# Kernel optimization log

Hardware: AMD Instinct MI355X
Metric: run time of the kernel (lower is better)

## Reference

```python
import jax, jax.numpy as jnp
import numpy as np
from jax import lax

P = 8  # patch size
DN = ('NCHW', 'OIHW', 'NCHW')

def setup_inputs() -> dict:
    key = jax.random.key(0)
    ks = jax.random.split(key, 8)
    B, D, H, W = 8, 64, 256, 256
    C = 4 * D
    return {
        'x': jax.random.normal(ks[0], (B, D, H, W), jnp.float32),
        'w_in': jax.random.normal(ks[1], (C, D, 1, 1), jnp.float32) * 0.05,
        'b_in': jax.random.normal(ks[2], (C,), jnp.float32) * 0.05,
        'fft_filter': jnp.ones((C, 1, 1, P, P // 2 + 1), jnp.float32),
        'w_dw': jax.random.normal(ks[3], (C, 1, 7, 7), jnp.float32) * 0.05,
        'b_dw': jax.random.normal(ks[4], (C,), jnp.float32) * 0.05,
        'w_out': jax.random.normal(ks[5], (D, C, 1, 1), jnp.float32) * 0.05,
        'b_out': jax.random.normal(ks[6], (D,), jnp.float32) * 0.05,
    }

def reference(x, w_in, b_in, fft_filter, w_dw, b_dw, w_out, b_out):
    B, D, H, W = x.shape
    C = w_in.shape[0]
    # conv_in: 1x1
    x = lax.conv_general_dilated(x, w_in, (1, 1), 'SAME', dimension_numbers=DN)
    x = x + b_in[None, :, None, None]
    # patchify: b c (h p1) (w p2) -> b c h w p1 p2
    xp = x.reshape(B, C, H // P, P, W // P, P).transpose(0, 1, 2, 4, 3, 5)
    # rfft2 over 8x8 patches (norm='backward' is default)
    xf = jnp.fft.rfft2(xp)
    # learned frequency filter (real), broadcasts over batch and patch grid
    xf = xf * fft_filter
    xp = jnp.fft.irfft2(xf, s=(P, P))
    # unpatchify
    x = xp.transpose(0, 1, 2, 4, 3, 5).reshape(B, C, H, W)
    # depthwise 7x7 conv
    x = lax.conv_general_dilated(x, w_dw, (1, 1), 'SAME',
                                 dimension_numbers=DN, feature_group_count=C)
    x = x + b_dw[None, :, None, None]
    x = jax.nn.gelu(x, approximate=False)
    # conv3: 1x1 back to dim
    x = lax.conv_general_dilated(x, w_out, (1, 1), 'SAME', dimension_numbers=DN)
    return x + b_out[None, :, None, None]
```

## Files before the change

kernel.cpp:

```cpp
#include <hip/hip_runtime.h>
#include <cstdint>
#include <cstddef>

#define HWSZ 65536

__device__ __forceinline__ uint32_t f2bfu(float f) {
  union { float f; uint32_t u; } v; v.f = f;
  return (v.u + 0x7FFFu + ((v.u >> 16) & 1u)) >> 16;
}
__device__ __forceinline__ float bfhi(uint32_t u) {
  union { uint32_t u; float f; } v; v.u = u & 0xffff0000u;
  return v.f;
}
__device__ __forceinline__ float bflo(uint32_t u) {
  union { uint32_t u; float f; } v; v.u = u << 16;
  return v.f;
}

__global__ void k_prep(const float* __restrict__ F, float* __restrict__ Ks) {
  __shared__ float ct[8];
  int t = threadIdx.x;
  int c = blockIdx.x;
  if (t == 0) {
    const float r2 = 0.70710678118654752f;
    ct[0] = 1.f; ct[1] = r2; ct[2] = 0.f; ct[3] = -r2;
    ct[4] = -1.f; ct[5] = -r2; ct[6] = 0.f; ct[7] = r2;
  }
  __syncthreads();
  int p = t >> 3, q = t & 7;
  const float* Fc = F + c * 40;
  float s = 0.f;
#pragma unroll
  for (int u = 0; u < 8; ++u) {
#pragma unroll
    for (int v = 0; v < 8; ++v) {
      float g = (v <= 4) ? Fc[u * 5 + v] : Fc[((8 - u) & 7) * 5 + (8 - v)];
      s += g * ct[(u * p + v * q) & 7];
    }
  }
  Ks[c * 64 + t] = s * (1.f / 64.f);
}

__global__ void k_wt(const float* __restrict__ w_out, float* __restrict__ wT) {
  int c = blockIdx.x;
  int d = threadIdx.x;
  wT[c * 64 + d] = w_out[d * 256 + c];
}

__global__ void k_wdw(const float* __restrict__ w_dw,
                      const float* __restrict__ b_dw,
                      float* __restrict__ wdwp) {
  int c = blockIdx.x;
  int t = threadIdx.x;
  int u = t >> 3, k = t & 7;
  float v = 0.f;
  if (t == 55) v = b_dw[c];
  else if (t < 56 && k < 7) v = w_dw[c * 49 + u * 7 + k];
  wdwp[c * 64 + t] = v;
}

__device__ __forceinline__ void circ8(const uint32_t* __restrict__ prb,
                                      const float* __restrict__ kc, int h,
                                      uint32_t* __restrict__ ou) {
  float o[32];
#pragma unroll
  for (int t = 0; t < 32; ++t) o[t] = 0.f;
#pragma unroll 1
  for (int tph = 0; tph < 2; ++tph) {
    float kh[32];
#pragma unroll
    for (int q4 = 0; q4 < 8; ++q4) {
      float4 kv = *(const float4*)(kc + tph * 32 + q4 * 4);
      kh[q4 * 4 + 0] = kv.x; kh[q4 * 4 + 1] = kv.y;
      kh[q4 * 4 + 2] = kv.z; kh[q4 * 4 + 3] = kv.w;
    }
#pragma unroll
    for (int ii = 0; ii < 4; ++ii) {
      int i = h * 4 + ii;
#pragma unroll
      for (int t4 = 0; t4 < 4; ++t4) {
        int tp = tph * 4 + t4;
        int r = (i - tp) & 7;
        uint2 ua = *(const uint2*)(prb + r * 4);
        uint2 ub = *(const uint2*)(prb + r * 4 + 2);
        float pr[8] = {bflo(ua.x), bfhi(ua.x), bflo(ua.y), bfhi(ua.y),
                       bflo(ub.x), bfhi(ub.x), bflo(ub.y), bfhi(ub.y)};
#pragma unroll
        for (int tq = 0; tq < 8; ++tq) {
          float kv = kh[t4 * 8 + tq];
#pragma unroll
          for (int j = 0; j < 8; ++j)
            o[ii * 8 + j] += kv * pr[(j - tq) & 7];
        }
      }
    }
  }
#pragma unroll
  for (int ii = 0; ii < 4; ++ii) {
    ou[ii * 4 + 0] = f2bfu(o[ii * 8 + 0]) | (f2bfu(o[ii * 8 + 1]) << 16);
    ou[ii * 4 + 1] = f2bfu(o[ii * 8 + 2]) | (f2bfu(o[ii * 8 + 3]) << 16);
    ou[ii * 4 + 2] = f2bfu(o[ii * 8 + 4]) | (f2bfu(o[ii * 8 + 5]) << 16);
    ou[ii * 4 + 3] = f2bfu(o[ii * 8 + 6]) | (f2bfu(o[ii * 8 + 7]) << 16);
  }
}

__global__ __launch_bounds__(256, 2) void k_front(
    const float* __restrict__ x, const float* __restrict__ w_in,
    const float* __restrict__ b_in, const float* __restrict__ Ks,
    uint32_t* __restrict__ midu) {
  __shared__ __align__(16) uint32_t Au[128 * 34];
  __shared__ __align__(16) uint32_t Bu[128 * 34];
  float* xs = (float*)Au;
  int tid = threadIdx.x;
  int orig = blockIdx.x;
  int pid = (orig & 7) * 1024 + (orig >> 3);
  int b = pid >> 10;
  int pp = pid & 1023;
  int ph = pp >> 5, pw = pp & 31;

  {
    const float* xb = x + (size_t)b * 64 * HWSZ + (ph * 8) * 256 + pw * 8;
#pragma unroll
    for (int k = 0; k < 4; ++k) {
      int s = tid + k * 256;
      int d = s >> 4, i = (s >> 1) & 7, jh = s & 1;
      float4 v = *(const float4*)(xb + (size_t)d * HWSZ + i * 256 + jh * 4);
      *(float4*)(xs + d * 64 + i * 8 + jh * 4) = v;
    }
  }
  int h = tid & 1;
  int cp = tid >> 1;
  int c0 = cp, c1 = cp + 128;
  float p0[32], p1[32];
  {
    float bi0 = b_in[c0], bi1 = b_in[c1];
#pragma unroll
    for (int t = 0; t < 32; ++t) { p0[t] = bi0; p1[t] = bi1; }
  }
  __syncthreads();

  const float* w0 = w_in + c0 * 64;
  const float* w1 = w_in + c1 * 64;
#pragma unroll 1
  for (int d8 = 0; d8 < 8; ++d8) {
    float4 wa0 = *(const float4*)(w0 + d8 * 8);
    float4 wb0 = *(const float4*)(w0 + d8 * 8 + 4);
    float4 wa1 = *(const float4*)(w1 + d8 * 8);
    float4 wb1 = *(const float4*)(w1 + d8 * 8 + 4);
    float wv0[8] = {wa0.x, wa0.y, wa0.z, wa0.w, wb0.x, wb0.y, wb0.z, wb0.w};
    float wv1[8] = {wa1.x, wa1.y, wa1.z, wa1.w, wb1.x, wb1.y, wb1.z, wb1.w};
#pragma unroll
    for (int dd = 0; dd < 8; ++dd) {
      const float4* xr = (const float4*)(xs + (d8 * 8 + dd) * 64 + h * 32);
#pragma unroll
      for (int t4 = 0; t4 < 8; ++t4) {
        float4 xv = xr[t4];
        p0[t4 * 4 + 0] += wv0[dd] * xv.x; p1[t4 * 4 + 0] += wv1[dd] * xv.x;
        p0[t4 * 4 + 1] += wv0[dd] * xv.y; p1[t4 * 4 + 1] += wv1[dd] * xv.y;
        p0[t4 * 4 + 2] += wv0[dd] * xv.z; p1[t4 * 4 + 2] += wv1[dd] * xv.z;
        p0[t4 * 4 + 3] += wv0[dd] * xv.w; p1[t4 * 4 + 3] += wv1[dd] * xv.w;
      }
    }
  }
  __syncthreads();

  {
    uint32_t* r0 = Au + c0 * 34 + h * 16;
    uint32_t* r1 = Bu + cp * 34 + h * 16;
#pragma unroll
    for (int ii = 0; ii < 4; ++ii) {
      uint2 ua, ub;
      ua.x = f2bfu(p0[ii * 8 + 0]) | (f2bfu(p0[ii * 8 + 1]) << 16);
      ua.y = f2bfu(p0[ii * 8 + 2]) | (f2bfu(p0[ii * 8 + 3]) << 16);
      ub.x = f2bfu(p0[ii * 8 + 4]) | (f2bfu(p0[ii * 8 + 5]) << 16);
      ub.y = f2bfu(p0[ii * 8 + 6]) | (f2bfu(p0[ii * 8 + 7]) << 16);
      *(uint2*)(r0 + ii * 4) = ua;
      *(uint2*)(r0 + ii * 4 + 2) = ub;
      ua.x = f2bfu(p1[ii * 8 + 0]) | (f2bfu(p1[ii * 8 + 1]) << 16);
      ua.y = f2bfu(p1[ii * 8 + 2]) | (f2bfu(p1[ii * 8 + 3]) << 16);
      ub.x = f2bfu(p1[ii * 8 + 4]) | (f2bfu(p1[ii * 8 + 5]) << 16);
      ub.y = f2bfu(p1[ii * 8 + 6]) | (f2bfu(p1[ii * 8 + 7]) << 16);
      *(uint2*)(r1 + ii * 4) = ua;
      *(uint2*)(r1 + ii * 4 + 2) = ub;
    }
  }
  __syncthreads();

  uint32_t ou[16];
  circ8(Au + c0 * 34, Ks + c0 * 64, h, ou);
  __syncthreads();
  {
    uint32_t* r0 = Au + c0 * 34 + h * 16;
#pragma unroll
    for (int m = 0; m < 4; ++m) {
      uint2 ua; ua.x = ou[m * 4 + 0]; ua.y = ou[m * 4 + 1];
      uint2 ub; ub.x = ou[m * 4 + 2]; ub.y = ou[m * 4 + 3];
      *(uint2*)(r0 + m * 4) = ua;
      *(uint2*)(r0 + m * 4 + 2) = ub;
    }
  }
  circ8(Bu + cp * 34, Ks + c1 * 64, h, ou);
  __syncthreads();
  {
    uint32_t* r1 = Bu + cp * 34 + h * 16;
#pragma unroll
    for (int m = 0; m < 4; ++m) {
      uint2 ua; ua.x = ou[m * 4 + 0]; ua.y = ou[m * 4 + 1];
      uint2 ub; ub.x = ou[m * 4 + 2]; ub.y = ou[m * 4 + 3];
      *(uint2*)(r1 + m * 4) = ua;
      *(uint2*)(r1 + m * 4 + 2) = ub;
    }
  }
  __syncthreads();

  uint32_t* gbase = midu + (size_t)(b * 1024 + pp) * 8192;
#pragma unroll
  for (int k = 0; k < 8; ++k) {
    int g = tid * 4 + k * 1024;
    int w = g & 31;
    uint2 a, e;
    if (k < 4) {
      int cc = g >> 5;
      a = *(uint2*)(Au + cc * 34 + w);
      e = *(uint2*)(Au + cc * 34 + w + 2);
    } else {
      int cc = (g >> 5) - 128;
      a = *(uint2*)(Bu + cc * 34 + w);
      e = *(uint2*)(Bu + cc * 34 + w + 2);
    }
    uint4 q; q.x = a.x; q.y = a.y; q.z = e.x; q.w = e.y;
    *(uint4*)(gbase + g) = q;
  }
}

#define TUB 48
__global__ __launch_bounds__(256, 1) void k_back(
    const uint32_t* __restrict__ midu, const float* __restrict__ wdwp,
    const float* __restrict__ wT, const float* __restrict__ b_out,
    float* __restrict__ out) {
  __shared__ __align__(16) uint32_t tile[2][22 * TUB];
  __shared__ __align__(16) float wbuf[2][128];
  int t = threadIdx.x;
  int orig = blockIdx.x;
  int pid = (orig & 7) * 128 + (orig >> 3);
  int b = pid >> 7;
  int tb = pid & 127;
  int th = tb >> 3, tw = tb & 7;
  int R0 = th * 16, C0 = tw * 32;

  for (int z = t; z < 2 * 22 * TUB; z += 256) ((uint32_t*)tile)[z] = 0u;

  int lr = t >> 3, p = t & 7;
  int g = R0 - 3 + lr;
  int pc = 4 * tw - 1 + p;
  bool aw = (t < 176) && (p < 6) && ((unsigned)g < 256u);
  bool qv = aw && ((unsigned)pc < 32u);
  size_t src0 = 0;
  if (qv)
    src0 = ((size_t)(b * 1024 + (g >> 3) * 32 + pc) * 8192) +
           (size_t)((g & 7) * 4);

  int ty = t >> 4, tx = t & 15;
  int lane = t - 192;

  float2 acc[64];
#pragma unroll
  for (int d = 0; d < 64; ++d) { acc[d].x = 0.f; acc[d].y = 0.f; }

  __syncthreads();

  {
    uint4 q; q.x = 0u; q.y = 0u; q.z = 0u; q.w = 0u;
    if (qv) q = *(const uint4*)(midu + src0);
    uint32_t ex = (uint32_t)__shfl_down((int)q.x, 1);
    if (aw) {
      uint32_t* dr = &tile[0][0] + lr * TUB;
      uint32_t w0 = (q.x >> 16) | (q.y << 16);
      uint32_t w1 = (q.y >> 16) | (q.z << 16);
      uint32_t w2 = (q.z >> 16) | (q.w << 16);
      uint32_t w3 = (q.w >> 16) | (ex << 16);
      if (p == 0) {
        uint2 hb; hb.x = w2; hb.y = w3;
        *(uint2*)(dr + 0) = hb;
      } else if (p == 5) {
        dr[18] = w0;
      } else {
        uint2 ha; ha.x = w0; ha.y = w1;
        uint2 hb; hb.x = w2; hb.y = w3;
        *(uint2*)(dr + 4 * p - 2) = ha;
        *(uint2*)(dr + 4 * p) = hb;
      }
    }
    if (t >= 192) {
      __builtin_amdgcn_global_load_lds(
          (const __attribute__((address_space(1))) uint32_t*)(wdwp + lane),
          (__attribute__((address_space(3))) uint32_t*)&wbuf[0][0], 4, 0, 0);
      __builtin_amdgcn_global_load_lds(
          (const __attribute__((address_space(1))) uint32_t*)(wT + lane),
          (__attribute__((address_space(3))) uint32_t*)&wbuf[0][64], 4, 0, 0);
    }
  }
  __syncthreads();

  for (int c = 0; c < 256; ++c) {
    int cur = c & 1;
    bool pf = (c < 255);
    uint4 q; q.x = 0u; q.y = 0u; q.z = 0u; q.w = 0u;
    if (pf && qv) q = *(const uint4*)(midu + src0 + (size_t)(c + 1) * 32);
    if (pf && t >= 192) {
      const float* wds = wdwp + (size_t)(c + 1) * 64 + lane;
      const float* wts = wT + (size_t)(c + 1) * 64 + lane;
      __builtin_amdgcn_global_load_lds(
          (const __attribute__((address_space(1))) uint32_t*)wds,
          (__attribute__((address_space(3))) uint32_t*)&wbuf[cur ^ 1][0],
          4, 0, 0);
      __builtin_amdgcn_global_load_lds(
          (const __attribute__((address_space(1))) uint32_t*)wts,
          (__attribute__((address_space(3))) uint32_t*)&wbuf[cur ^ 1][64],
          4, 0, 0);
    }

    const uint32_t* tl = &tile[cur][0];
    const float* wl = wbuf[cur];
    float s0 = wl[55], s1 = s0;
#pragma unroll
    for (int u = 0; u < 7; ++u) {
      const uint32_t* row = tl + (ty + u) * TUB + tx;
      uint32_t k0 = row[0], k1 = row[1], k2 = row[2], k3 = row[3];
      float f0 = bflo(k0), f1 = bfhi(k0), f2 = bflo(k1), f3 = bfhi(k1);
      float f4 = bflo(k2), f5 = bfhi(k2), f6 = bflo(k3), f7 = bfhi(k3);
      float4 wA = *(const float4*)(wl + u * 8);
      float4 wB = *(const float4*)(wl + u * 8 + 4);
      s0 += wA.x * f0 + wA.y * f1 + wA.z * f2 + wA.w * f3 + wB.x * f4 +
            wB.y * f5 + wB.z * f6;
      s1 += wA.x * f1 + wA.y * f2 + wA.z * f3 + wA.w * f4 + wB.x * f5 +
            wB.y * f6 + wB.z * f7;
    }
    const float RS2 = 0.70710678118654752f;
    float g0 = 0.5f * s0 * (1.f + erff(s0 * RS2));
    float g1 = 0.5f * s1 * (1.f + erff(s1 * RS2));

    const float* wcl = wl + 64;
#pragma unroll
    for (int d4 = 0; d4 < 16; ++d4) {
      float4 wv = *(const float4*)(wcl + d4 * 4);
      acc[d4 * 4 + 0].x += g0 * wv.x; acc[d4 * 4 + 0].y += g1 * wv.x;
      acc[d4 * 4 + 1].x += g0 * wv.y; acc[d4 * 4 + 1].y += g1 * wv.y;
      acc[d4 * 4 + 2].x += g0 * wv.z; acc[d4 * 4 + 2].y += g1 * wv.z;
      acc[d4 * 4 + 3].x += g0 * wv.w; acc[d4 * 4 + 3].y += g1 * wv.w;
    }

    if (pf) {
      uint32_t ex = (uint32_t)__shfl_down((int)q.x, 1);
      if (aw) {
        uint32_t* dr = &tile[cur ^ 1][0] + lr * TUB;
        uint32_t w0 = (q.x >> 16) | (q.y << 16);
        uint32_t w1 = (q.y >> 16) | (q.z << 16);
        uint32_t w2 = (q.z >> 16) | (q.w << 16);
        uint32_t w3 = (q.w >> 16) | (ex << 16);
        if (p == 0) {
          uint2 hb; hb.x = w2; hb.y = w3;
          *(uint2*)(dr + 0) = hb;
        } else if (p == 5) {
          dr[18] = w0;
        } else {
          uint2 ha; ha.x = w0; ha.y = w1;
          uint2 hb; hb.x = w2; hb.y = w3;
          *(uint2*)(dr + 4 * p - 2) = ha;
          *(uint2*)(dr + 4 * p) = hb;
        }
      }
    }
    __syncthreads();
  }

  size_t obase = (size_t)b * 64 * HWSZ + (size_t)(R0 + ty) * 256 + C0 + 2 * tx;
#pragma unroll
  for (int d = 0; d < 64; ++d) {
    float bo = b_out[d];
    float2 v; v.x = acc[d].x + bo; v.y = acc[d].y + bo;
    *(float2*)(out + obase + (size_t)d * HWSZ) = v;
  }
}

extern "C" void kernel_launch(void* const* d_in, const int* in_sizes, int n_in,
                              void* d_out, int out_size, void* d_ws, size_t ws_size,
                              hipStream_t stream) {
  (void)in_sizes; (void)n_in; (void)out_size; (void)ws_size;
  const float* x     = (const float*)d_in[0];
  const float* w_in  = (const float*)d_in[1];
  const float* b_in  = (const float*)d_in[2];
  const float* fftf  = (const float*)d_in[3];
  const float* w_dw  = (const float*)d_in[4];
  const float* b_dw  = (const float*)d_in[5];
  const float* w_out = (const float*)d_in[6];
  const float* b_out = (const float*)d_in[7];
  float* out = (float*)d_out;

  float* Ks = (float*)d_ws;
  float* wT = (float*)((char*)d_ws + 65536);
  float* wdwp = (float*)((char*)d_ws + 131072);
  uint32_t* midu = (uint32_t*)((char*)d_ws + 196608);

  k_prep<<<256, 64, 0, stream>>>(fftf, Ks);
  k_wt<<<256, 64, 0, stream>>>(w_out, wT);
  k_wdw<<<256, 64, 0, stream>>>(w_dw, b_dw, wdwp);
  k_front<<<8192, 256, 0, stream>>>(x, w_in, b_in, Ks, midu);
  k_back<<<1024, 256, 0, stream>>>(midu, wdwp, wT, b_out, out);
}
```

Baseline: 1.381 ms.

## Stream back-kernel tiles via async global-to-LDS loads with 8-deep channel ring

Replaces the register-staged global load plus shift/repack of the bf16 tile with direct global_load_lds copies of 4-byte words into a compact 24-word row layout, reading one extra word per row instead of shuffling halves. Channels are now processed in groups of four with an eight-slot LDS ring buffer, so the next four channels are prefetched while the current four compute and a barrier is needed only once per group. This removes per-channel VGPR staging, shuffles and barriers, and uses more LDS.

```diff
diff --git a/kernel.cpp b/kernel.cpp
--- a/kernel.cpp
+++ b/kernel.cpp
@@ -233,13 +233,14 @@
   }
 }
 
-#define TUB 48
+#define TST 24
+#define TEL 528
 __global__ __launch_bounds__(256, 1) void k_back(
     const uint32_t* __restrict__ midu, const float* __restrict__ wdwp,
     const float* __restrict__ wT, const float* __restrict__ b_out,
     float* __restrict__ out) {
-  __shared__ __align__(16) uint32_t tile[2][22 * TUB];
-  __shared__ __align__(16) float wbuf[2][128];
+  __shared__ __align__(16) uint32_t T[8][TEL];
+  __shared__ __align__(16) float wbuf[8][128];
   int t = threadIdx.x;
   int orig = blockIdx.x;
   int pid = (orig & 7) * 128 + (orig >> 3);
@@ -248,127 +249,131 @@
   int th = tb >> 3, tw = tb & 7;
   int R0 = th * 16, C0 = tw * 32;
 
-  for (int z = t; z < 2 * 22 * TUB; z += 256) ((uint32_t*)tile)[z] = 0u;
-
-  int lr = t >> 3, p = t & 7;
-  int g = R0 - 3 + lr;
-  int pc = 4 * tw - 1 + p;
-  bool aw = (t < 176) && (p < 6) && ((unsigned)g < 256u);
-  bool qv = aw && ((unsigned)pc < 32u);
-  size_t src0 = 0;
-  if (qv)
-    src0 = ((size_t)(b * 1024 + (g >> 3) * 32 + pc) * 8192) +
-           (size_t)((g & 7) * 4);
+  uint32_t off1 = 0, off2 = 0, off3 = 0;
+  bool v1, v2, v3;
+  {
+    int e1 = t, e2 = 256 + t;
+    int r1 = e1 / 24, j1 = e1 % 24;
+    int r2 = e2 / 24, j2 = e2 % 24;
+    int r3 = 21, j3 = 8 + t;
+    int gg, p0, pc, w;
+    gg = R0 - 3 + r1; p0 = C0 - 4 + 2 * j1; pc = p0 >> 3; w = (p0 & 7) >> 1;
+    v1 = (j1 < 20) && ((unsigned)gg < 256u) && ((unsigned)pc < 32u);
+    if (v1) off1 = ((uint32_t)(b * 1024 + (gg >> 3) * 32 + pc) * 8192u +
+                    (uint32_t)((gg & 7) * 4 + w)) * 4u;
+    gg = R0 - 3 + r2; p0 = C0 - 4 + 2 * j2; pc = p0 >> 3; w = (p0 & 7) >> 1;
+    v2 = (j2 < 20) && ((unsigned)gg < 256u) && ((unsigned)pc < 32u);
+    if (v2) off2 = ((uint32_t)(b * 1024 + (gg >> 3) * 32 + pc) * 8192u +
+                    (uint32_t)((gg & 7) * 4 + w)) * 4u;
+    gg = R0 - 3 + r3; p0 = C0 - 4 + 2 * j3; pc = p0 >> 3; w = (p0 & 7) >> 1;
+    v3 = (j3 < 20) && ((unsigned)gg < 256u) && ((unsigned)pc < 32u);
+    if (v3) off3 = ((uint32_t)(b * 1024 + (gg >> 3) * 32 + pc) * 8192u +
+                    (uint32_t)((gg & 7) * 4 + w)) * 4u;
+  }
+  int wb = t & 192;
+  int lane = t - 192;
 
   int ty = t >> 4, tx = t & 15;
-  int lane = t - 192;
 
   float2 acc[64];
 #pragma unroll
   for (int d = 0; d < 64; ++d) { acc[d].x = 0.f; acc[d].y = 0.f; }
 
-  __syncthreads();
-
-  {
-    uint4 q; q.x = 0u; q.y = 0u; q.z = 0u; q.w = 0u;
-    if (qv) q = *(const uint4*)(midu + src0);
-    uint32_t ex = (uint32_t)__shfl_down((int)q.x, 1);
-    if (aw) {
-      uint32_t* dr = &tile[0][0] + lr * TUB;
-      uint32_t w0 = (q.x >> 16) | (q.y << 16);
-      uint32_t w1 = (q.y >> 16) | (q.z << 16);
-      uint32_t w2 = (q.z >> 16) | (q.w << 16);
-      uint32_t w3 = (q.w >> 16) | (ex << 16);
-      if (p == 0) {
-        uint2 hb; hb.x = w2; hb.y = w3;
-        *(uint2*)(dr + 0) = hb;
-      } else if (p == 5) {
-        dr[18] = w0;
-      } else {
-        uint2 ha; ha.x = w0; ha.y = w1;
-        uint2 hb; hb.x = w2; hb.y = w3;
-        *(uint2*)(dr + 4 * p - 2) = ha;
-        *(uint2*)(dr + 4 * p) = hb;
-      }
-    }
+  for (int z = t; z < 8 * TEL; z += 256) ((uint32_t*)T)[z] = 0u;
+  __syncthreads();
+
+#pragma unroll
+  for (int s = 0; s < 4; ++s) {
+    const char* mb = (const char*)midu + (size_t)s * 128u;
+    if (v1) __builtin_amdgcn_global_load_lds(
+        (const __attribute__((address_space(1))) uint32_t*)(mb + off1),
+        (__attribute__((address_space(3))) uint32_t*)&T[s][wb], 4, 0, 0);
+    if (v2) __builtin_amdgcn_global_load_lds(
+        (const __attribute__((address_space(1))) uint32_t*)(mb + off2),
+        (__attribute__((address_space(3))) uint32_t*)&T[s][256 + wb], 4, 0, 0);
+    if (v3) __builtin_amdgcn_global_load_lds(
+        (const __attribute__((address_space(1))) uint32_t*)(mb + off3),
+        (__attribute__((address_space(3))) uint32_t*)&T[s][512], 4, 0, 0);
     if (t >= 192) {
       __builtin_amdgcn_global_load_lds(
-          (const __attribute__((address_space(1))) uint32_t*)(wdwp + lane),
-          (__attribute__((address_space(3))) uint32_t*)&wbuf[0][0], 4, 0, 0);
+          (const __attribute__((address_space(1))) uint32_t*)
+              (wdwp + s * 64 + lane),
+          (__attribute__((address_space(3))) uint32_t*)&wbuf[s][0], 4, 0, 0);
       __builtin_amdgcn_global_load_lds(
-          (const __attribute__((address_space(1))) uint32_t*)(wT + lane),
-          (__attribute__((address_space(3))) uint32_t*)&wbuf[0][64], 4, 0, 0);
-    }
-  }
-  __syncthreads();
-
-  for (int c = 0; c < 256; ++c) {
-    int cur = c & 1;
-    bool pf = (c < 255);
-    uint4 q; q.x = 0u; q.y = 0u; q.z = 0u; q.w = 0u;
-    if (pf && qv) q = *(const uint4*)(midu + src0 + (size_t)(c + 1) * 32);
-    if (pf && t >= 192) {
-      const float* wds = wdwp + (size_t)(c + 1) * 64 + lane;
-      const float* wts = wT + (size_t)(c + 1) * 64 + lane;
-      __builtin_amdgcn_global_load_lds(
-          (const __attribute__((address_space(1))) uint32_t*)wds,
-          (__attribute__((address_space(3))) uint32_t*)&wbuf[cur ^ 1][0],
-          4, 0, 0);
-      __builtin_amdgcn_global_load_lds(
-          (const __attribute__((address_space(1))) uint32_t*)wts,
-          (__attribute__((address_space(3))) uint32_t*)&wbuf[cur ^ 1][64],
-          4, 0, 0);
-    }
-
-    const uint32_t* tl = &tile[cur][0];
-    const float* wl = wbuf[cur];
-    float s0 = wl[55], s1 = s0;
-#pragma unroll
-    for (int u = 0; u < 7; ++u) {
-      const uint32_t* row = tl + (ty + u) * TUB + tx;
-      uint32_t k0 = row[0], k1 = row[1], k2 = row[2], k3 = row[3];
-      float f0 = bflo(k0), f1 = bfhi(k0), f2 = bflo(k1), f3 = bfhi(k1);
-      float f4 = bflo(k2), f5 = bfhi(k2), f6 = bflo(k3), f7 = bfhi(k3);
-      float4 wA = *(const float4*)(wl + u * 8);
-      float4 wB = *(const float4*)(wl + u * 8 + 4);
-      s0 += wA.x * f0 + wA.y * f1 + wA.z * f2 + wA.w * f3 + wB.x * f4 +
-            wB.y * f5 + wB.z * f6;
-      s1 += wA.x * f1 + wA.y * f2 + wA.z * f3 + wA.w * f4 + wB.x * f5 +
-            wB.y * f6 + wB.z * f7;
-    }
-    const float RS2 = 0.70710678118654752f;
-    float g0 = 0.5f * s0 * (1.f + erff(s0 * RS2));
-    float g1 = 0.5f * s1 * (1.f + erff(s1 * RS2));
-
-    const float* wcl = wl + 64;
-#pragma unroll
-    for (int d4 = 0; d4 < 16; ++d4) {
-      float4 wv = *(const float4*)(wcl + d4 * 4);
-      acc[d4 * 4 + 0].x += g0 * wv.x; acc[d4 * 4 + 0].y += g1 * wv.x;
-      acc[d4 * 4 + 1].x += g0 * wv.y; acc[d4 * 4 + 1].y += g1 * wv.y;
-      acc[d4 * 4 + 2].x += g0 * wv.z; acc[d4 * 4 + 2].y += g1 * wv.z;
-      acc[d4 * 4 + 3].x += g0 * wv.w; acc[d4 * 4 + 3].y += g1 * wv.w;
-    }
-
-    if (pf) {
-      uint32_t ex = (uint32_t)__shfl_down((int)q.x, 1);
-      if (aw) {
-        uint32_t* dr = &tile[cur ^ 1][0] + lr * TUB;
-        uint32_t w0 = (q.x >> 16) | (q.y << 16);
-        uint32_t w1 = (q.y >> 16) | (q.z << 16);
-        uint32_t w2 = (q.z >> 16) | (q.w << 16);
-        uint32_t w3 = (q.w >> 16) | (ex << 16);
-        if (p == 0) {
-          uint2 hb; hb.x = w2; hb.y = w3;
-          *(uint2*)(dr + 0) = hb;
-        } else if (p == 5) {
-          dr[18] = w0;
-        } else {
-          uint2 ha; ha.x = w0; ha.y = w1;
-          uint2 hb; hb.x = w2; hb.y = w3;
-          *(uint2*)(dr + 4 * p - 2) = ha;
-          *(uint2*)(dr + 4 * p) = hb;
+          (const __attribute__((address_space(1))) uint32_t*)
+              (wT + s * 64 + lane),
+          (__attribute__((address_space(3))) uint32_t*)&wbuf[s][64], 4, 0, 0);
+    }
+  }
+  __syncthreads();
+
+  for (int c = 0; c < 256; c += 4) {
+    if (c < 252) {
+#pragma unroll
+      for (int s = 0; s < 4; ++s) {
+        int ch = c + 4 + s;
+        int bi = ch & 7;
+        const char* mb = (const char*)midu + (size_t)ch * 128u;
+        if (v1) __builtin_amdgcn_global_load_lds(
+            (const __attribute__((address_space(1))) uint32_t*)(mb + off1),
+            (__attribute__((address_space(3))) uint32_t*)&T[bi][wb], 4, 0, 0);
+        if (v2) __builtin_amdgcn_global_load_lds(
+            (const __attribute__((address_space(1))) uint32_t*)(mb + off2),
+            (__attribute__((address_space(3))) uint32_t*)&T[bi][256 + wb],
+            4, 0, 0);
+        if (v3) __builtin_amdgcn_global_load_lds(
+            (const __attribute__((address_space(1))) uint32_t*)(mb + off3),
+            (__attribute__((address_space(3))) uint32_t*)&T[bi][512], 4, 0, 0);
+        if (t >= 192) {
+          __builtin_amdgcn_global_load_lds(
+              (const __attribute__((address_space(1))) uint32_t*)
+                  (wdwp + ch * 64 + lane),
+              (__attribute__((address_space(3))) uint32_t*)&wbuf[bi][0],
+              4, 0, 0);
+          __builtin_amdgcn_global_load_lds(
+              (const __attribute__((address_space(1))) uint32_t*)
+                  (wT + ch * 64 + lane),
+              (__attribute__((address_space(3))) uint32_t*)&wbuf[bi][64],
+              4, 0, 0);
         }
+      }
+    }
+
+#pragma unroll 1
+    for (int k = 0; k < 4; ++k) {
+      int bi = (c + k) & 7;
+      const uint32_t* tl = &T[bi][0];
+      const float* wl = &wbuf[bi][0];
+      float s0 = wl[55], s1 = s0;
+#pragma unroll
+      for (int u = 0; u < 7; ++u) {
+        const uint32_t* row = tl + (ty + u) * TST + tx;
+        uint32_t k0 = row[0], k1 = row[1], k2 = row[2], k3 = row[3];
+        uint32_t k4 = row[4];
+        float f0 = bfhi(k0);
+        float f1 = bflo(k1), f2 = bfhi(k1);
+        float f3 = bflo(k2), f4 = bfhi(k2);
+        float f5 = bflo(k3), f6 = bfhi(k3);
+        float f7 = bflo(k4);
+        float4 wA = *(const float4*)(wl + u * 8);
+        float4 wB = *(const float4*)(wl + u * 8 + 4);
+        s0 += wA.x * f0 + wA.y * f1 + wA.z * f2 + wA.w * f3 + wB.x * f4 +
+              wB.y * f5 + wB.z * f6;
+        s1 += wA.x * f1 + wA.y * f2 + wA.z * f3 + wA.w * f4 + wB.x * f5 +
+              wB.y * f6 + wB.z * f7;
+      }
+      const float RS2 = 0.70710678118654752f;
+      float g0 = 0.5f * s0 * (1.f + erff(s0 * RS2));
+      float g1 = 0.5f * s1 * (1.f + erff(s1 * RS2));
+
+      const float* wcl = wl + 64;
+#pragma unroll
+      for (int d4 = 0; d4 < 16; ++d4) {
+        float4 wv = *(const float4*)(wcl + d4 * 4);
+        acc[d4 * 4 + 0].x += g0 * wv.x; acc[d4 * 4 + 0].y += g1 * wv.x;
+        acc[d4 * 4 + 1].x += g0 * wv.y; acc[d4 * 4 + 1].y += g1 * wv.y;
+        acc[d4 * 4 + 2].x += g0 * wv.z; acc[d4 * 4 + 2].y += g1 * wv.z;
+        acc[d4 * 4 + 3].x += g0 * wv.w; acc[d4 * 4 + 3].y += g1 * wv.w;
       }
     }
     __syncthreads();
```

Result: slower. 1.456 ms (+5.5%).
